# Performance work log

Measured on AMD Instinct MI355X. Metric: run time of the kernel, lower is better.

The kernel has to match this reference:

```python
import jax, jax.numpy as jnp
import numpy as np

N_NODES = 100000
N_REL = 8
N_EDGES = 80000
IN_F, HID, OUT = 128, 32, 2
N_GRAPHS = 64


def setup_inputs() -> dict:
    key = jax.random.key(0)
    ks = jax.random.split(key, 12)
    x = jax.random.normal(ks[0], (N_NODES, IN_F), dtype=jnp.float32)
    src = jax.random.randint(ks[1], (N_REL, N_EDGES), 0, N_NODES, dtype=jnp.int32)
    dst = jax.random.randint(ks[2], (N_REL, N_EDGES), 0, N_NODES, dtype=jnp.int32)
    graph_ids = jax.random.randint(ks[3], (N_NODES,), 0, N_GRAPHS, dtype=jnp.int32)
    W1 = jax.random.normal(ks[4], (N_REL, IN_F, HID), dtype=jnp.float32) / np.sqrt(IN_F)
    b1 = jnp.zeros((N_REL, HID), dtype=jnp.float32)
    W2 = jax.random.normal(ks[5], (N_REL, HID, HID), dtype=jnp.float32) / np.sqrt(HID)
    b2 = jnp.zeros((N_REL, HID), dtype=jnp.float32)
    Wc = jax.random.normal(ks[6], (HID, OUT), dtype=jnp.float32) / np.sqrt(HID)
    bc = jnp.zeros((OUT,), dtype=jnp.float32)
    return {"x": x, "src": src, "dst": dst, "graph_ids": graph_ids,
            "num_graphs": N_GRAPHS, "W1": W1, "b1": b1, "W2": W2, "b2": b2,
            "Wc": Wc, "bc": bc}


def _hetero_conv(h, src, dst, W, b, n_nodes):
    """HeteroGraphConv(sum) of per-relation GraphConv(norm='both')."""
    n_rel = W.shape[0]
    out = jnp.zeros((n_nodes, W.shape[2]), dtype=h.dtype)
    ones_e = jnp.ones((src.shape[1],), dtype=h.dtype)
    for r in range(n_rel):  # small fixed relation set
        s, d = src[r], dst[r]
        # symmetric normalization with degree clamped to >= 1 (DGL behavior)
        deg_out = jnp.maximum(jax.ops.segment_sum(ones_e, s, num_segments=n_nodes), 1.0)
        deg_in = jnp.maximum(jax.ops.segment_sum(ones_e, d, num_segments=n_nodes), 1.0)
        hn = h * jax.lax.rsqrt(deg_out)[:, None]      # [N, F_in]
        hw = hn @ W[r]                                # project first (F_in >= F_out)
        agg = jax.ops.segment_sum(hw[s], d, num_segments=n_nodes)  # scatter-sum to dst
        out = out + agg * jax.lax.rsqrt(deg_in)[:, None] + b[r]
    return out


def reference(x, src, dst, graph_ids, num_graphs, W1, b1, W2, b2, Wc, bc):
    n = x.shape[0]
    h = jax.nn.relu(_hetero_conv(x, src, dst, W1, b1, n))
    h = _hetero_conv(h, src, dst, W2, b2, n)
    # per-graph mean pooling over nodes
    sums = jax.ops.segment_sum(h, graph_ids, num_segments=num_graphs)
    cnts = jnp.maximum(jax.ops.segment_sum(jnp.ones((n,), h.dtype), graph_ids,
                                           num_segments=num_graphs), 1.0)
    pooled = sums / cnts[:, None]
    return pooled @ Wc + bc
```

## Files before the change

### kernel.cpp

```cpp
#include <hip/hip_runtime.h>


#define N_NODES 100000
#define N_REL   8
#define N_EDGES 80000
#define IN_F    128
#define HID     32
#define N_GRAPHS 64
#define NCAT    (N_REL * HID)
#define N_KEYS  (N_NODES * N_REL)
#define TOT_E   (N_REL * N_EDGES)
#define DEG_BLOCKS  (TOT_E / 256)
#define GEMM_BLOCKS ((N_NODES / 16 + 3) / 4)

constexpr int TILE = 256;
constexpr int KC   = 32;

typedef __attribute__((ext_vector_type(8))) short bf16x8;
typedef __attribute__((ext_vector_type(4))) float f32x4;

__device__ __forceinline__ ushort f2bf(float v) {
  unsigned u = __builtin_bit_cast(unsigned, v);
  u = (u + 0x7fffu + ((u >> 16) & 1u)) >> 16;
  return (ushort)u;
}
__device__ __forceinline__ float bf2f(ushort h) {
  unsigned u = ((unsigned)h) << 16;
  return __builtin_bit_cast(float, u);
}

__global__ __launch_bounds__(256) void rsqrt_kernel(float* __restrict__ p, int count) {
  int i = blockIdx.x * 256 + threadIdx.x;
  if (i < count) {
    int d = ((const int*)p)[i];
    p[i] = rsqrtf((float)(d < 1 ? 1 : d));
  }
}

__global__ __launch_bounds__(256) void prep_w_kernel(const float* __restrict__ W1, const float* __restrict__ W2,
                                                     const float* __restrict__ Wc,
                                                     ushort* __restrict__ Wt1, ushort* __restrict__ Vt) {
  int i = blockIdx.x * 256 + threadIdx.x;
  if (i < NCAT * IN_F) {
    int n = i >> 7, k = i & 127;
    int r = n >> 5, j = n & 31;
    Wt1[i] = f2bf(W1[r * (IN_F * HID) + k * HID + j]);
  } else {
    int q = i - NCAT * IN_F;
    if (q < 16 * HID) {
      int n = q >> 5, k = q & 31;
      int r = n >> 1, c = n & 1;
      float s = 0.f;
#pragma unroll
      for (int j = 0; j < HID; j++) s += W2[r * (HID * HID) + k * HID + j] * Wc[j * 2 + c];
      Vt[q] = f2bf(s);
    }
  }
}

__global__ __launch_bounds__(256, 4) void fused_deg_gemm1(const int* __restrict__ src, const int* __restrict__ dst,
                                                          int* __restrict__ dego, int* __restrict__ cnt,
                                                          int* __restrict__ epos,
                                                          const float* __restrict__ A, const ushort* __restrict__ Bt,
                                                          ushort* __restrict__ Y, int M) {
  __shared__ ushort smem[17408];
  int bid = blockIdx.x;
  int isg, rid;
  if (bid < 2 * GEMM_BLOCKS) { isg = !(bid & 1); rid = bid >> 1; }
  else { isg = 0; rid = GEMM_BLOCKS + (bid - 2 * GEMM_BLOCKS); }

  if (!isg) {
    int i = rid * 256 + (int)threadIdx.x;
    int s = src[i], d = dst[i];
    int r = i / N_EDGES;
    atomicAdd(&dego[r * N_NODES + s], 1);
    epos[i] = atomicAdd(&cnt[d * N_REL + r], 1);
    return;
  }

  int wave = __builtin_amdgcn_readfirstlane(threadIdx.x >> 6);
  int lane = threadIdx.x & 63;
  int t = threadIdx.x;
  int m0 = (rid * 4 + wave) * 16;
  int me = (m0 <= M - 16) ? m0 : (M - 16);
  int row = lane & 15, quad = lane >> 4;

  bf16x8 af[4];
#pragma unroll
  for (int kq = 0; kq < 4; kq++) {
    const float* ap = &A[(size_t)(me + row) * IN_F + kq * 32 + quad * 8];
    float4 a0 = *(const float4*)ap;
    float4 a1 = *(const float4*)(ap + 4);
    bf16x8 a;
    a[0] = (short)f2bf(a0.x); a[1] = (short)f2bf(a0.y); a[2] = (short)f2bf(a0.z); a[3] = (short)f2bf(a0.w);
    a[4] = (short)f2bf(a1.x); a[5] = (short)f2bf(a1.y); a[6] = (short)f2bf(a1.z); a[7] = (short)f2bf(a1.w);
    af[kq] = a;
  }

  f32x4 acc[16];
#pragma unroll
  for (int nt = 0; nt < 16; nt++) acc[nt] = (f32x4){0.f, 0.f, 0.f, 0.f};

  for (int p = 0; p < 2; p++) {
    __syncthreads();
    const ushort* bsrc = Bt + (size_t)p * (128 * IN_F);
#pragma unroll
    for (int i = 0; i < 8; i++) {
      int c = t + i * 256;
      int rr2 = c >> 4, cc = c & 15;
      uint4 v = *(const uint4*)&bsrc[rr2 * IN_F + cc * 8];
      *(uint4*)&smem[rr2 * 136 + cc * 8] = v;
    }
    __syncthreads();
#pragma unroll
    for (int kq = 0; kq < 4; kq++) {
#pragma unroll
      for (int nt2 = 0; nt2 < 8; nt2++) {
        bf16x8 b = *(const bf16x8*)&smem[(nt2 * 16 + row) * 136 + kq * 32 + quad * 8];
        acc[p * 8 + nt2] = __builtin_amdgcn_mfma_f32_16x16x32_bf16(af[kq], b, acc[p * 8 + nt2], 0, 0, 0);
      }
    }
  }
  __syncthreads();

  ushort* myt = &smem[wave * 4160];
#pragma unroll
  for (int nt = 0; nt < 16; nt++) {
#pragma unroll
    for (int i = 0; i < 4; i++)
      myt[(quad * 4 + i) * 260 + nt * 16 + row] = f2bf(acc[nt][i]);
  }
  if (m0 <= M - 16) {
    ushort* ybase = &Y[(size_t)m0 * NCAT];
#pragma unroll
    for (int k = 0; k < 8; k++) {
      int g = k * 512 + lane * 8;
      int r2 = g >> 8, c2 = g & 255;
      const ushort* sp = &myt[r2 * 260 + c2];
      uint4 v;
      v.x = *(const uint*)(sp + 0);
      v.y = *(const uint*)(sp + 2);
      v.z = *(const uint*)(sp + 4);
      v.w = *(const uint*)(sp + 6);
      *(uint4*)&ybase[g] = v;
    }
  }
}

__global__ __launch_bounds__(256) void scan1_kernel(const int* __restrict__ in, int* __restrict__ out,
                                                    int* __restrict__ partial, int n) {
  __shared__ int ts[256];
  int b0 = blockIdx.x * 1024;
  int t = threadIdx.x;
  int v[4]; int s = 0;
#pragma unroll
  for (int k = 0; k < 4; k++) {
    int idx = b0 + t * 4 + k;
    v[k] = s;
    s += (idx < n) ? in[idx] : 0;
  }
  ts[t] = s;
  __syncthreads();
  for (int off = 1; off < 256; off <<= 1) {
    int xv = (t >= off) ? ts[t - off] : 0;
    __syncthreads();
    ts[t] += xv;
    __syncthreads();
  }
  int texcl = (t == 0) ? 0 : ts[t - 1];
#pragma unroll
  for (int k = 0; k < 4; k++) {
    int idx = b0 + t * 4 + k;
    if (idx < n) out[idx] = texcl + v[k];
  }
  if (t == 255) {
    partial[blockIdx.x] = ts[255];
    if (b0 + 1024 >= n) out[n] = ts[255];
  }
}

__global__ __launch_bounds__(256) void scan2_kernel(int* __restrict__ partial, int nb) {
  __shared__ int ts[256];
  int t = threadIdx.x;
  int v[4]; int s = 0;
#pragma unroll
  for (int k = 0; k < 4; k++) {
    int idx = t * 4 + k;
    v[k] = s;
    s += (idx < nb) ? partial[idx] : 0;
  }
  ts[t] = s;
  __syncthreads();
  for (int off = 1; off < 256; off <<= 1) {
    int xv = (t >= off) ? ts[t - off] : 0;
    __syncthreads();
    ts[t] += xv;
    __syncthreads();
  }
  int texcl = (t == 0) ? 0 : ts[t - 1];
#pragma unroll
  for (int k = 0; k < 4; k++) {
    int idx = t * 4 + k;
    if (idx < nb) partial[idx] = texcl + v[k];
  }
}

__global__ __launch_bounds__(256) void fill_kernel(const int* __restrict__ src, const int* __restrict__ dst,
                                                   const int* __restrict__ rp, const int* __restrict__ part,
                                                   const int* __restrict__ epos, const int* __restrict__ dego,
                                                   int2* __restrict__ edata) {
  int i = blockIdx.x * 256 + threadIdx.x;
  int d = dst[i];
  int s = src[i];
  int r = i / N_EDGES;
  int key = d * N_REL + r;
  int b = rp[key] + part[key >> 10];
  int k1 = key + 1;
  int e2 = rp[k1] + part[k1 >> 10];
  int c = e2 - b;
  int t = b + epos[i];
  int dg = dego[r * N_NODES + s];
  float w = rsqrtf((float)(dg < 1 ? 1 : dg)) * rsqrtf((float)(c < 1 ? 1 : c));
  int2 e;
  e.x = s * NCAT + r * HID;
  e.y = __builtin_bit_cast(int, w);
  edata[t] = e;
}

__global__ __launch_bounds__(256) void gather1_kernel(const ushort* __restrict__ Ys, const int2* __restrict__ edata,
                                                      const int* __restrict__ rp, const int* __restrict__ part,
                                                      const float* __restrict__ b1, const ushort* __restrict__ Vt,
                                                      float* __restrict__ Ys2) {
  int wave = __builtin_amdgcn_readfirstlane(threadIdx.x >> 6);
  int lane = threadIdx.x & 63;
  int d = blockIdx.x * 4 + wave;
  if (d >= N_NODES) return;
  int j = lane & 31, half = lane >> 5;
  int k0 = d * N_REL, k1 = k0 + N_REL;
  int base = rp[k0] + part[k0 >> 10];
  int endp = rp[k1] + part[k1 >> 10];
  float sum = 0.f;
  for (int t = base + half; t < endp; t += 2) {
    int2 e = edata[t];
    float w = __builtin_bit_cast(float, e.y);
    sum += w * bf2f(Ys[(size_t)e.x + j]);
  }
  sum += __shfl_down(sum, 32);
  float sb = 0.f;
#pragma unroll
  for (int q = 0; q < N_REL; q++) sb += b1[q * HID + j];
  float h = fmaxf(sum + sb, 0.f);
  bf16x8 vrow[4];
  if (lane < 16) {
#pragma unroll
    for (int q = 0; q < 4; q++) vrow[q] = *(const bf16x8*)&Vt[lane * HID + q * 8];
  } else {
#pragma unroll
    for (int q = 0; q < 4; q++) vrow[q] = (bf16x8){0,0,0,0,0,0,0,0};
  }
  float acc = 0.f;
#pragma unroll
  for (int jj = 0; jj < 32; jj++) {
    float hv = __shfl(h, jj);
    acc += hv * bf2f((ushort)vrow[jj >> 3][jj & 7]);
  }
  if (lane < 16) Ys2[(size_t)d * 16 + lane] = acc;
}

__global__ __launch_bounds__(256) void gather2_pool_kernel(const float* __restrict__ Ys2,
                                                           const int2* __restrict__ edata,
                                                           const int* __restrict__ rp, const int* __restrict__ part,
                                                           const int* __restrict__ gid,
                                                           float* __restrict__ gpool, float* __restrict__ gcnt) {
  __shared__ float lp[N_GRAPHS * 2];
  __shared__ float lc[N_GRAPHS];
  int t = threadIdx.x;
  if (t < N_GRAPHS * 2) lp[t] = 0.f;
  if (t < N_GRAPHS) lc[t] = 0.f;
  __syncthreads();
  for (int n = blockIdx.x * 256 + t; n < N_NODES; n += gridDim.x * 256) {
    int k0 = n * N_REL, k1 = k0 + N_REL;
    int base = rp[k0] + part[k0 >> 10];
    int endp = rp[k1] + part[k1 >> 10];
    float z0 = 0.f, z1 = 0.f;
    for (int s = base; s < endp; s++) {
      int2 e = edata[s];
      float w = __builtin_bit_cast(float, e.y);
      float2 y = *(const float2*)&Ys2[e.x >> 4];
      z0 += w * y.x;
      z1 += w * y.y;
    }
    int g = gid[n];
    atomicAdd(&lp[g * 2 + 0], z0);
    atomicAdd(&lp[g * 2 + 1], z1);
    atomicAdd(&lc[g], 1.f);
  }
  __syncthreads();
  if (t < N_GRAPHS * 2) atomicAdd(&gpool[t], lp[t]);
  if (t < N_GRAPHS) atomicAdd(&gcnt[t], lc[t]);
}

__global__ void final_kernel(const float* __restrict__ gpool, const float* __restrict__ gcnt,
                             const float* __restrict__ b2, const float* __restrict__ Wc,
                             const float* __restrict__ bc, float* __restrict__ out) {
  int g = threadIdx.x;
  if (g >= N_GRAPHS) return;
  float c0 = 0.f, c1 = 0.f;
#pragma unroll
  for (int k = 0; k < HID; k++) {
    float sb = 0.f;
#pragma unroll
    for (int r = 0; r < N_REL; r++) sb += b2[r * HID + k];
    c0 += sb * Wc[k * 2 + 0];
    c1 += sb * Wc[k * 2 + 1];
  }
  float cntv = gcnt[g];
  if (cntv > 0.f) {
    out[g * 2 + 0] = gpool[g * 2 + 0] / cntv + c0 + bc[0];
    out[g * 2 + 1] = gpool[g * 2 + 1] / cntv + c1 + bc[1];
  } else {
    out[g * 2 + 0] = bc[0];
    out[g * 2 + 1] = bc[1];
  }
}

__global__ __launch_bounds__(256) void deg_kernel(const int* __restrict__ src, const int* __restrict__ dst,
                                                  int* __restrict__ dego, int* __restrict__ degi, int n_rel) {
  int i = blockIdx.x * 256 + threadIdx.x;
  if (i < n_rel * N_EDGES) {
    int r = i / N_EDGES;
    atomicAdd(&dego[r * N_NODES + src[i]], 1);
    atomicAdd(&degi[r * N_NODES + dst[i]], 1);
  }
}

__global__ __launch_bounds__(256) void proj1_kernel(const float* __restrict__ x, const float* __restrict__ W1r0,
                                                    const float* __restrict__ rs_o, float* __restrict__ hw,
                                                    int n0, int n1, int hw_nodes) {
  int rr = blockIdx.y;
  int nb = n0 + blockIdx.x * TILE;
  int t = threadIdx.x;
  __shared__ float xs[TILE][KC + 4];
  const float* __restrict__ Wr = W1r0 + (size_t)rr * (IN_F * HID);
  float acc[HID];
#pragma unroll
  for (int j = 0; j < HID; j++) acc[j] = 0.f;
  for (int kc = 0; kc < IN_F; kc += KC) {
    __syncthreads();
#pragma unroll
    for (int i = 0; i < (TILE * KC / 4) / 256; i++) {
      int q = t + i * 256;
      int nn = q >> 3, k4 = q & 7;
      int n = nb + nn;
      float4 v = make_float4(0.f, 0.f, 0.f, 0.f);
      if (n < n1) v = *(const float4*)&x[(size_t)n * IN_F + kc + k4 * 4];
      *(float4*)&xs[nn][k4 * 4] = v;
    }
    __syncthreads();
#pragma unroll
    for (int k4 = 0; k4 < KC / 4; k4++) {
      float4 xv = *(const float4*)&xs[t][k4 * 4];
      const float* wk = &Wr[(kc + k4 * 4) * HID];
#pragma unroll
      for (int j = 0; j < HID; j++) acc[j] += xv.x * wk[j];
#pragma unroll
      for (int j = 0; j < HID; j++) acc[j] += xv.y * wk[HID + j];
#pragma unroll
      for (int j = 0; j < HID; j++) acc[j] += xv.z * wk[2 * HID + j];
#pragma unroll
      for (int j = 0; j < HID; j++) acc[j] += xv.w * wk[3 * HID + j];
    }
  }
  int n = nb + t;
  if (n < n1) {
    float s = rs_o[(size_t)rr * N_NODES + n];
    float* o = &hw[((size_t)rr * hw_nodes + (n - n0)) * HID];
#pragma unroll
    for (int j4 = 0; j4 < HID / 4; j4++) {
      float4 v = make_float4(acc[j4 * 4] * s, acc[j4 * 4 + 1] * s, acc[j4 * 4 + 2] * s, acc[j4 * 4 + 3] * s);
      *(float4*)&o[j4 * 4] = v;
    }
  }
}

__global__ __launch_bounds__(256) void proj2_kernel(const float* __restrict__ acc1, const float* __restrict__ b1,
                                                    const float* __restrict__ W2r0, const float* __restrict__ rs_o,
                                                    float* __restrict__ hw, int n0, int n1, int hw_nodes) {
  int n = n0 + blockIdx.x * 256 + threadIdx.x;
  if (n >= n1) return;
  int rr = blockIdx.y;
  float h1[HID];
#pragma unroll
  for (int j4 = 0; j4 < HID / 4; j4++) {
    float4 v = *(const float4*)&acc1[(size_t)n * HID + j4 * 4];
    h1[j4 * 4 + 0] = v.x; h1[j4 * 4 + 1] = v.y; h1[j4 * 4 + 2] = v.z; h1[j4 * 4 + 3] = v.w;
  }
#pragma unroll
  for (int j = 0; j < HID; j++) {
    float sb = 0.f;
#pragma unroll
    for (int q = 0; q < N_REL; q++) sb += b1[q * HID + j];
    h1[j] = fmaxf(h1[j] + sb, 0.f);
  }
  const float* __restrict__ Wr = W2r0 + (size_t)rr * (HID * HID);
  float acc[HID];
#pragma unroll
  for (int j = 0; j < HID; j++) acc[j] = 0.f;
#pragma unroll
  for (int k = 0; k < HID; k++) {
    float hv = h1[k];
#pragma unroll
    for (int j = 0; j < HID; j++) acc[j] += hv * Wr[k * HID + j];
  }
  float s = rs_o[(size_t)rr * N_NODES + n];
  float* o = &hw[((size_t)rr * hw_nodes + (n - n0)) * HID];
#pragma unroll
  for (int j4 = 0; j4 < HID / 4; j4++) {
    float4 v = make_float4(acc[j4 * 4] * s, acc[j4 * 4 + 1] * s, acc[j4 * 4 + 2] * s, acc[j4 * 4 + 3] * s);
    *(float4*)&o[j4 * 4] = v;
  }
}

__global__ __launch_bounds__(256) void scatter_kernel(const float* __restrict__ hw, const int* __restrict__ src,
                                                      const int* __restrict__ dst, const float* __restrict__ rs_i,
                                                      float* __restrict__ acc, int nr, int n0, int n1, int hw_nodes) {
  long i = (long)blockIdx.x * 256 + threadIdx.x;
  long total = (long)nr * N_EDGES * HID;
  if (i >= total) return;
  int j = (int)(i & (HID - 1));
  long e = i >> 5;
  int rr = (int)(e / N_EDGES);
  int ee = (int)(e - (long)rr * N_EDGES);
  int s = src[rr * N_EDGES + ee];
  if (s < n0 || s >= n1) return;
  int d = dst[rr * N_EDGES + ee];
  float v = hw[((size_t)rr * hw_nodes + (s - n0)) * HID + j] * rs_i[(size_t)rr * N_NODES + d];
  atomicAdd(&acc[(size_t)d * HID + j], v);
}

__global__ __launch_bounds__(256) void pool_kernel(const float* __restrict__ acc2, const float* __restrict__ b2,
                                                   const int* __restrict__ gid, float* __restrict__ gpool,
                                                   float* __restrict__ gcnt) {
  __shared__ float lp[N_GRAPHS * HID];
  __shared__ float lc[N_GRAPHS];
  int t = threadIdx.x;
  for (int i = t; i < N_GRAPHS * HID; i += 256) lp[i] = 0.f;
  if (t < N_GRAPHS) lc[t] = 0.f;
  __syncthreads();
  int j = t & (HID - 1);
  int grp = t >> 5;
  float sb = 0.f;
#pragma unroll
  for (int q = 0; q < N_REL; q++) sb += b2[q * HID + j];
  for (int n = blockIdx.x * 8 + grp; n < N_NODES; n += gridDim.x * 8) {
    int g = gid[n];
    float v = acc2[(size_t)n * HID + j] + sb;
    atomicAdd(&lp[g * HID + j], v);
    if (j == 0) atomicAdd(&lc[g], 1.f);
  }
  __syncthreads();
  for (int i = t; i < N_GRAPHS * HID; i += 256) atomicAdd(&gpool[i], lp[i]);
  if (t < N_GRAPHS) atomicAdd(&gcnt[t], lc[t]);
}

__global__ void final3_kernel(const float* __restrict__ gpool, const float* __restrict__ gcnt,
                              const float* __restrict__ Wc, const float* __restrict__ bc,
                              float* __restrict__ out) {
  int g = threadIdx.x;
  if (g >= N_GRAPHS) return;
  float inv = 1.f / fmaxf(gcnt[g], 1.f);
  float o0 = bc[0], o1 = bc[1];
#pragma unroll
  for (int k = 0; k < HID; k++) {
    float p = gpool[g * HID + k] * inv;
    o0 += p * Wc[k * 2 + 0];
    o1 += p * Wc[k * 2 + 1];
  }
  out[g * 2 + 0] = o0;
  out[g * 2 + 1] = o1;
}

extern "C" void kernel_launch(void* const* d_in, const int* in_sizes, int n_in,
                              void* d_out, int out_size, void* d_ws, size_t ws_size,
                              hipStream_t stream) {
  const float* x  = (const float*)d_in[0];
  const int* src  = (const int*)d_in[1];
  const int* dst  = (const int*)d_in[2];
  const int* gid  = (const int*)d_in[3];
  const float* W1 = (const float*)d_in[5];
  const float* b1 = (const float*)d_in[6];
  const float* W2 = (const float*)d_in[7];
  const float* b2 = (const float*)d_in[8];
  const float* Wc = (const float*)d_in[9];
  const float* bc = (const float*)d_in[10];
  float* out = (float*)d_out;

  float* ws = (float*)d_ws;
  const size_t NF = (size_t)N_NODES * HID;
  const size_t RN = (size_t)N_REL * N_NODES;
  const size_t POOLF = N_GRAPHS * HID + N_GRAPHS;
  size_t wsf = ws_size / 4;

  const size_t T1_NEED = 22500000;

  if (wsf >= T1_NEED) {
    float* gpool = ws;
    float* gcnt  = gpool + N_GRAPHS * 2;
    int*   dego  = (int*)(gcnt + N_GRAPHS);
    int*   cnt   = dego + RN;
    int*   epos  = cnt + N_KEYS;
    int*   rp    = epos + TOT_E;
    int*   part  = rp + N_KEYS + 8;
    int2*  edata = (int2*)(part + 1024);
    float* Ys2   = (float*)(edata + TOT_E);
    ushort* Ys   = (ushort*)(Ys2 + (size_t)N_NODES * 16);
    ushort* Wt1  = Ys + (size_t)N_NODES * NCAT;
    ushort* Vt   = Wt1 + NCAT * IN_F;

    size_t zbytes = (N_GRAPHS * 3 + RN + (size_t)N_KEYS) * 4;
    hipMemsetAsync(ws, 0, zbytes, stream);

    prep_w_kernel<<<(NCAT * IN_F + 16 * HID + 255) / 256, 256, 0, stream>>>(W1, W2, Wc, Wt1, Vt);
    fused_deg_gemm1<<<DEG_BLOCKS + GEMM_BLOCKS, 256, 0, stream>>>(src, dst, dego, cnt, epos,
                                                                  x, Wt1, Ys, N_NODES);

    int sblocks = (N_KEYS + 1023) / 1024;
    scan1_kernel<<<sblocks, 256, 0, stream>>>(cnt, rp, part, N_KEYS);
    scan2_kernel<<<1, 256, 0, stream>>>(part, sblocks);
    fill_kernel<<<TOT_E / 256, 256, 0, stream>>>(src, dst, rp, part, epos, dego, edata);

    int nblocks = (N_NODES + 3) / 4;
    gather1_kernel<<<nblocks, 256, 0, stream>>>(Ys, edata, rp, part, b1, Vt, Ys2);
    gather2_pool_kernel<<<416, 256, 0, stream>>>(Ys2, edata, rp, part, gid, gpool, gcnt);
    final_kernel<<<1, 64, 0, stream>>>(gpool, gcnt, b2, Wc, bc, out);
  } else {
    float* acc1  = ws;
    float* acc2  = acc1 + NF;
    float* gpool = acc2 + NF;
    float* gcnt  = gpool + N_GRAPHS * HID;
    float* rsb   = ws + (2 * NF + POOLF);
    size_t zf = 2 * NF + POOLF;
    float* rs_o = rsb;
    float* rs_i = rsb + N_NODES;
    float* hw = rsb + 2 * N_NODES;
    size_t fixed3 = zf + 2 * N_NODES;
    size_t avail = (wsf > fixed3) ? (wsf - fixed3) : 0;
    long chunk = (long)(avail / HID) & ~255L;
    if (chunk < 256) chunk = 256;
    if (chunk > N_NODES) chunk = N_NODES;

    size_t zb = zf * 4; if (zb > ws_size) zb = ws_size;
    hipMemsetAsync(d_ws, 0, zb, stream);

    for (int layer = 0; layer < 2; layer++) {
      for (int r = 0; r < N_REL; r++) {
        hipMemsetAsync(rs_o, 0, 2 * N_NODES * 4, stream);
        deg_kernel<<<(N_EDGES + 255) / 256, 256, 0, stream>>>(src + (size_t)r * N_EDGES, dst + (size_t)r * N_EDGES,
                                                              (int*)rs_o, (int*)rs_i, 1);
        rsqrt_kernel<<<(2 * N_NODES + 255) / 256, 256, 0, stream>>>(rs_o, 2 * N_NODES);
        for (long n0 = 0; n0 < N_NODES; n0 += chunk) {
          long n1 = n0 + chunk; if (n1 > N_NODES) n1 = N_NODES;
          int tiles = (int)((n1 - n0 + TILE - 1) / TILE);
          if (layer == 0)
            proj1_kernel<<<dim3(tiles, 1), 256, 0, stream>>>(x, W1 + (size_t)r * IN_F * HID, rs_o, hw,
                                                             (int)n0, (int)n1, (int)chunk);
          else
            proj2_kernel<<<dim3(tiles, 1), 256, 0, stream>>>(acc1, b1, W2 + (size_t)r * HID * HID, rs_o, hw,
                                                             (int)n0, (int)n1, (int)chunk);
          long tot = (long)N_EDGES * HID;
          scatter_kernel<<<(int)((tot + 255) / 256), 256, 0, stream>>>(hw, src + (size_t)r * N_EDGES,
                                                                       dst + (size_t)r * N_EDGES, rs_i,
                                                                       layer == 0 ? acc1 : acc2,
                                                                       1, (int)n0, (int)n1, (int)chunk);
        }
      }
    }
    pool_kernel<<<256, 256, 0, stream>>>(acc2, b2, gid, gpool, gcnt);
    final3_kernel<<<1, 64, 0, stream>>>(gpool, gcnt, Wc, bc, out);
  }
}
```

Baseline: 259.2 us.

## Pipeline edge fill and first gather across destination-node ranges

Splits the CSR fill and the layer-1 gather into three destination-node ranges. Each launch fills the next range's edges while gathering the previous range, with fill and gather blocks interleaved. This is meant to overlap the latency-bound fill with the gather and hide launch gaps. The cost is that every fill pass rereads all edges (three full scans of dst) and there are more kernel launches.

Result: slower. 267.8 us (+3.3%).

```diff
diff --git a/kernel.cpp b/kernel.cpp
--- a/kernel.cpp
+++ b/kernel.cpp
@@ -12,6 +12,9 @@
 #define TOT_E   (N_REL * N_EDGES)
 #define DEG_BLOCKS  (TOT_E / 256)
 #define GEMM_BLOCKS ((N_NODES / 16 + 3) / 4)
+#define FILL_BLOCKS (TOT_E / 256)
+#define DCUT1 33334
+#define DCUT2 66667
 
 constexpr int TILE = 256;
 constexpr int KC   = 32;
@@ -205,12 +208,13 @@
   }
 }
 
-__global__ __launch_bounds__(256) void fill_kernel(const int* __restrict__ src, const int* __restrict__ dst,
-                                                   const int* __restrict__ rp, const int* __restrict__ part,
-                                                   const int* __restrict__ epos, const int* __restrict__ dego,
-                                                   int2* __restrict__ edata) {
-  int i = blockIdx.x * 256 + threadIdx.x;
+__device__ __forceinline__ void fill_body(int i, int d0, int d1,
+                                          const int* __restrict__ src, const int* __restrict__ dst,
+                                          const int* __restrict__ rp, const int* __restrict__ part,
+                                          const int* __restrict__ epos, const int* __restrict__ dego,
+                                          int2* __restrict__ edata) {
   int d = dst[i];
+  if (d < d0 || d >= d1) return;
   int s = src[i];
   int r = i / N_EDGES;
   int key = d * N_REL + r;
@@ -227,14 +231,11 @@
   edata[t] = e;
 }
 
-__global__ __launch_bounds__(256) void gather1_kernel(const ushort* __restrict__ Ys, const int2* __restrict__ edata,
-                                                      const int* __restrict__ rp, const int* __restrict__ part,
-                                                      const float* __restrict__ b1, const ushort* __restrict__ Vt,
-                                                      float* __restrict__ Ys2) {
-  int wave = __builtin_amdgcn_readfirstlane(threadIdx.x >> 6);
-  int lane = threadIdx.x & 63;
-  int d = blockIdx.x * 4 + wave;
-  if (d >= N_NODES) return;
+__device__ __forceinline__ void g1_body(int d, int lane,
+                                        const ushort* __restrict__ Ys, const int2* __restrict__ edata,
+                                        const int* __restrict__ rp, const int* __restrict__ part,
+                                        const float* __restrict__ b1, const ushort* __restrict__ Vt,
+                                        float* __restrict__ Ys2) {
   int j = lane & 31, half = lane >> 5;
   int k0 = d * N_REL, k1 = k0 + N_REL;
   int base = rp[k0] + part[k0 >> 10];
@@ -265,6 +266,49 @@
     acc += hv * bf2f((ushort)vrow[jj >> 3][jj & 7]);
   }
   if (lane < 16) Ys2[(size_t)d * 16 + lane] = acc;
+}
+
+__global__ __launch_bounds__(256) void fill_kernel(const int* __restrict__ src, const int* __restrict__ dst,
+                                                   const int* __restrict__ rp, const int* __restrict__ part,
+                                                   const int* __restrict__ epos, const int* __restrict__ dego,
+                                                   int2* __restrict__ edata, int d0, int d1) {
+  int i = blockIdx.x * 256 + threadIdx.x;
+  fill_body(i, d0, d1, src, dst, rp, part, epos, dego, edata);
+}
+
+__global__ __launch_bounds__(256) void gather1_kernel(const ushort* __restrict__ Ys, const int2* __restrict__ edata,
+                                                      const int* __restrict__ rp, const int* __restrict__ part,
+                                                      const float* __restrict__ b1, const ushort* __restrict__ Vt,
+                                                      float* __restrict__ Ys2, int n0, int n1) {
+  int wave = __builtin_amdgcn_readfirstlane(threadIdx.x >> 6);
+  int lane = threadIdx.x & 63;
+  int d = n0 + blockIdx.x * 4 + wave;
+  if (d >= n1) return;
+  g1_body(d, lane, Ys, edata, rp, part, b1, Vt, Ys2);
+}
+
+__global__ __launch_bounds__(256) void fused_fill_g1(const int* __restrict__ src, const int* __restrict__ dst,
+                                                     const int* __restrict__ rp, const int* __restrict__ part,
+                                                     const int* __restrict__ epos, const int* __restrict__ dego,
+                                                     int2* __restrict__ edata, int fd0, int fd1,
+                                                     const ushort* __restrict__ Ys,
+                                                     const float* __restrict__ b1, const ushort* __restrict__ Vt,
+                                                     float* __restrict__ Ys2, int n0, int n1) {
+  int bid = blockIdx.x;
+  int isf, rid;
+  if (bid < 2 * FILL_BLOCKS) { isf = !(bid & 1); rid = bid >> 1; }
+  else { isf = 0; rid = FILL_BLOCKS + (bid - 2 * FILL_BLOCKS); }
+
+  if (isf) {
+    int i = rid * 256 + (int)threadIdx.x;
+    fill_body(i, fd0, fd1, src, dst, rp, part, epos, dego, edata);
+    return;
+  }
+  int wave = __builtin_amdgcn_readfirstlane(threadIdx.x >> 6);
+  int lane = threadIdx.x & 63;
+  int d = n0 + rid * 4 + wave;
+  if (d >= n1) return;
+  g1_body(d, lane, Ys, edata, rp, part, b1, Vt, Ys2);
 }
 
 __global__ __launch_bounds__(256) void gather2_pool_kernel(const float* __restrict__ Ys2,
@@ -527,10 +571,23 @@
     int sblocks = (N_KEYS + 1023) / 1024;
     scan1_kernel<<<sblocks, 256, 0, stream>>>(cnt, rp, part, N_KEYS);
     scan2_kernel<<<1, 256, 0, stream>>>(part, sblocks);
-    fill_kernel<<<TOT_E / 256, 256, 0, stream>>>(src, dst, rp, part, epos, dego, edata);
-
-    int nblocks = (N_NODES + 3) / 4;
-    gather1_kernel<<<nblocks, 256, 0, stream>>>(Ys, edata, rp, part, b1, Vt, Ys2);
+
+    fill_kernel<<<FILL_BLOCKS, 256, 0, stream>>>(src, dst, rp, part, epos, dego, edata, 0, DCUT1);
+    {
+      int g1b = (DCUT1 + 3) / 4;
+      fused_fill_g1<<<FILL_BLOCKS + g1b, 256, 0, stream>>>(src, dst, rp, part, epos, dego, edata,
+                                                           DCUT1, DCUT2,
+                                                           Ys, b1, Vt, Ys2, 0, DCUT1);
+    }
+    {
+      int g1b = (DCUT2 - DCUT1 + 3) / 4;
+      fused_fill_g1<<<FILL_BLOCKS + g1b, 256, 0, stream>>>(src, dst, rp, part, epos, dego, edata,
+                                                           DCUT2, N_NODES,
+                                                           Ys, b1, Vt, Ys2, DCUT1, DCUT2);
+    }
+    gather1_kernel<<<(N_NODES - DCUT2 + 3) / 4, 256, 0, stream>>>(Ys, edata, rp, part, b1, Vt, Ys2,
+                                                                  DCUT2, N_NODES);
+
     gather2_pool_kernel<<<416, 256, 0, stream>>>(Ys2, edata, rp, part, gid, gpool, gcnt);
     final_kernel<<<1, 64, 0, stream>>>(gpool, gcnt, b2, Wc, bc, out);
   } else {
```

## Flatten pooling gather to per-edge loop and move graph counts into fused kernel

Applied to the files above, without the earlier changes.

The second-layer gather and pool now iterate over all edges directly, using a destination id stored in a widened edge record. This replaces per-node CSR loops that have uneven trip counts. Per-graph node counts are computed by extra blocks in the fused degree/GEMM kernel instead of inside the pooling loop. The change balances work across threads, but doubles the edge record size read by fill and gather1 and puts many more shared-memory atomics on only 128 pool slots.

Result: no change. 258.7 us (-0.2%).

```diff
diff --git a/kernel.cpp b/kernel.cpp
--- a/kernel.cpp
+++ b/kernel.cpp
@@ -12,6 +12,7 @@
 #define TOT_E   (N_REL * N_EDGES)
 #define DEG_BLOCKS  (TOT_E / 256)
 #define GEMM_BLOCKS ((N_NODES / 16 + 3) / 4)
+#define GID_BLOCKS  ((N_NODES + 1023) / 1024)
 
 constexpr int TILE = 256;
 constexpr int KC   = 32;
@@ -62,19 +63,36 @@
                                                           int* __restrict__ dego, int* __restrict__ cnt,
                                                           int* __restrict__ epos,
                                                           const float* __restrict__ A, const ushort* __restrict__ Bt,
-                                                          ushort* __restrict__ Y, int M) {
+                                                          ushort* __restrict__ Y, int M,
+                                                          const int* __restrict__ gid, float* __restrict__ gcnt) {
   __shared__ ushort smem[17408];
   int bid = blockIdx.x;
-  int isg, rid;
-  if (bid < 2 * GEMM_BLOCKS) { isg = !(bid & 1); rid = bid >> 1; }
-  else { isg = 0; rid = GEMM_BLOCKS + (bid - 2 * GEMM_BLOCKS); }
-
-  if (!isg) {
+  int role, rid;
+  if (bid < 2 * GEMM_BLOCKS) { role = bid & 1; rid = bid >> 1; }
+  else if (bid < GEMM_BLOCKS + DEG_BLOCKS) { role = 1; rid = GEMM_BLOCKS + (bid - 2 * GEMM_BLOCKS); }
+  else { role = 2; rid = bid - (GEMM_BLOCKS + DEG_BLOCKS); }
+
+  if (role == 1) {
     int i = rid * 256 + (int)threadIdx.x;
     int s = src[i], d = dst[i];
     int r = i / N_EDGES;
     atomicAdd(&dego[r * N_NODES + s], 1);
     epos[i] = atomicAdd(&cnt[d * N_REL + r], 1);
+    return;
+  }
+  if (role == 2) {
+    int* gh = (int*)smem;
+    int t = threadIdx.x;
+    if (t < N_GRAPHS) gh[t] = 0;
+    __syncthreads();
+    int base = rid * 1024;
+#pragma unroll
+    for (int k = 0; k < 4; k++) {
+      int n = base + k * 256 + t;
+      if (n < N_NODES) atomicAdd(&gh[gid[n]], 1);
+    }
+    __syncthreads();
+    if (t < N_GRAPHS) atomicAdd(&gcnt[t], (float)gh[t]);
     return;
   }
 
@@ -208,7 +226,7 @@
 __global__ __launch_bounds__(256) void fill_kernel(const int* __restrict__ src, const int* __restrict__ dst,
                                                    const int* __restrict__ rp, const int* __restrict__ part,
                                                    const int* __restrict__ epos, const int* __restrict__ dego,
-                                                   int2* __restrict__ edata) {
+                                                   int4* __restrict__ edata) {
   int i = blockIdx.x * 256 + threadIdx.x;
   int d = dst[i];
   int s = src[i];
@@ -221,13 +239,15 @@
   int t = b + epos[i];
   int dg = dego[r * N_NODES + s];
   float w = rsqrtf((float)(dg < 1 ? 1 : dg)) * rsqrtf((float)(c < 1 ? 1 : c));
-  int2 e;
+  int4 e;
   e.x = s * NCAT + r * HID;
   e.y = __builtin_bit_cast(int, w);
+  e.z = d;
+  e.w = 0;
   edata[t] = e;
 }
 
-__global__ __launch_bounds__(256) void gather1_kernel(const ushort* __restrict__ Ys, const int2* __restrict__ edata,
+__global__ __launch_bounds__(256) void gather1_kernel(const ushort* __restrict__ Ys, const int4* __restrict__ edata,
                                                       const int* __restrict__ rp, const int* __restrict__ part,
                                                       const float* __restrict__ b1, const ushort* __restrict__ Vt,
                                                       float* __restrict__ Ys2) {
@@ -241,7 +261,7 @@
   int endp = rp[k1] + part[k1 >> 10];
   float sum = 0.f;
   for (int t = base + half; t < endp; t += 2) {
-    int2 e = edata[t];
+    int4 e = edata[t];
     float w = __builtin_bit_cast(float, e.y);
     sum += w * bf2f(Ys[(size_t)e.x + j]);
   }
@@ -268,36 +288,23 @@
 }
 
 __global__ __launch_bounds__(256) void gather2_pool_kernel(const float* __restrict__ Ys2,
-                                                           const int2* __restrict__ edata,
-                                                           const int* __restrict__ rp, const int* __restrict__ part,
+                                                           const int4* __restrict__ edata,
                                                            const int* __restrict__ gid,
-                                                           float* __restrict__ gpool, float* __restrict__ gcnt) {
+                                                           float* __restrict__ gpool) {
   __shared__ float lp[N_GRAPHS * 2];
-  __shared__ float lc[N_GRAPHS];
   int t = threadIdx.x;
   if (t < N_GRAPHS * 2) lp[t] = 0.f;
-  if (t < N_GRAPHS) lc[t] = 0.f;
-  __syncthreads();
-  for (int n = blockIdx.x * 256 + t; n < N_NODES; n += gridDim.x * 256) {
-    int k0 = n * N_REL, k1 = k0 + N_REL;
-    int base = rp[k0] + part[k0 >> 10];
-    int endp = rp[k1] + part[k1 >> 10];
-    float z0 = 0.f, z1 = 0.f;
-    for (int s = base; s < endp; s++) {
-      int2 e = edata[s];
-      float w = __builtin_bit_cast(float, e.y);
-      float2 y = *(const float2*)&Ys2[e.x >> 4];
-      z0 += w * y.x;
-      z1 += w * y.y;
-    }
-    int g = gid[n];
-    atomicAdd(&lp[g * 2 + 0], z0);
-    atomicAdd(&lp[g * 2 + 1], z1);
-    atomicAdd(&lc[g], 1.f);
+  __syncthreads();
+  for (int sidx = blockIdx.x * 256 + t; sidx < TOT_E; sidx += gridDim.x * 256) {
+    int4 e = edata[sidx];
+    float w = __builtin_bit_cast(float, e.y);
+    float2 y = *(const float2*)&Ys2[e.x >> 4];
+    int g = gid[e.z];
+    atomicAdd(&lp[g * 2 + 0], w * y.x);
+    atomicAdd(&lp[g * 2 + 1], w * y.y);
   }
   __syncthreads();
   if (t < N_GRAPHS * 2) atomicAdd(&gpool[t], lp[t]);
-  if (t < N_GRAPHS) atomicAdd(&gcnt[t], lc[t]);
 }
 
 __global__ void final_kernel(const float* __restrict__ gpool, const float* __restrict__ gcnt,
@@ -511,7 +518,7 @@
     int*   epos  = cnt + N_KEYS;
     int*   rp    = epos + TOT_E;
     int*   part  = rp + N_KEYS + 8;
-    int2*  edata = (int2*)(part + 1024);
+    int4*  edata = (int4*)(part + 1024);
     float* Ys2   = (float*)(edata + TOT_E);
     ushort* Ys   = (ushort*)(Ys2 + (size_t)N_NODES * 16);
     ushort* Wt1  = Ys + (size_t)N_NODES * NCAT;
@@ -521,8 +528,8 @@
     hipMemsetAsync(ws, 0, zbytes, stream);
 
     prep_w_kernel<<<(NCAT * IN_F + 16 * HID + 255) / 256, 256, 0, stream>>>(W1, W2, Wc, Wt1, Vt);
-    fused_deg_gemm1<<<DEG_BLOCKS + GEMM_BLOCKS, 256, 0, stream>>>(src, dst, dego, cnt, epos,
-                                                                  x, Wt1, Ys, N_NODES);
+    fused_deg_gemm1<<<DEG_BLOCKS + GEMM_BLOCKS + GID_BLOCKS, 256, 0, stream>>>(src, dst, dego, cnt, epos,
+                                                                               x, Wt1, Ys, N_NODES, gid, gcnt);
 
     int sblocks = (N_KEYS + 1023) / 1024;
     scan1_kernel<<<sblocks, 256, 0, stream>>>(cnt, rp, part, N_KEYS);
@@ -531,7 +538,7 @@
 
     int nblocks = (N_NODES + 3) / 4;
     gather1_kernel<<<nblocks, 256, 0, stream>>>(Ys, edata, rp, part, b1, Vt, Ys2);
-    gather2_pool_kernel<<<416, 256, 0, stream>>>(Ys2, edata, rp, part, gid, gpool, gcnt);
+    gather2_pool_kernel<<<416, 256, 0, stream>>>(Ys2, edata, gid, gpool);
     final_kernel<<<1, 64, 0, stream>>>(gpool, gcnt, b2, Wc, bc, out);
   } else {
     float* acc1  = ws;
```
